# Performance work log

Measured on AMD Instinct MI355X. Metric: run time of the kernel, lower is better.

Reference implementation:

```python
import jax, jax.numpy as jnp
import numpy as np

CH = 256          # channels
K = 3             # kernel_size
GROUP_CH = 16
G = CH // GROUP_CH   # groups = 16
RED = 2              # red_ratio
PAD = (K - 1) // 2
B, H, W = 8, 64, 64  # input must be spatially square (h==w) because the
                     # original forward does kernel @ x_unfolded over (h,w)


def setup_inputs() -> dict:
    key = jax.random.key(0)
    k1, k2, k3 = jax.random.split(key, 3)
    x = jax.random.normal(k1, (B, CH, H, W), dtype=jnp.float32)
    W_reduce = jax.random.normal(k2, (CH // RED, CH), dtype=jnp.float32) * 0.05
    b_reduce = jnp.zeros((CH // RED,), dtype=jnp.float32)
    W_span = jax.random.normal(k3, (K * K * G, CH // RED), dtype=jnp.float32) * 0.05
    b_span = jnp.zeros((K * K * G,), dtype=jnp.float32)
    return {"x": x, "W_reduce": W_reduce, "b_reduce": b_reduce,
            "W_span": W_span, "b_span": b_span}


def _unfold(x):
    """torch.nn.Unfold(K, dilation=1, padding=PAD, stride=1).
    Returns [b, c, K*K, h, w] with kernel positions in row-major order,
    channel-major overall (matches torch's C*K^2 flattening)."""
    b, c, h, w = x.shape
    xp = jnp.pad(x, ((0, 0), (0, 0), (PAD, PAD), (PAD, PAD)))
    patches = jnp.stack(
        [xp[:, :, ki:ki + h, kj:kj + w] for ki in range(K) for kj in range(K)],
        axis=2)
    return patches


def reference(x, W_reduce, b_reduce, W_span, b_span):
    b, c, h, w = x.shape
    # stride == 1 -> self.out is Identity
    red = jnp.einsum('bchw,oc->bohw', x, W_reduce) + b_reduce[None, :, None, None]
    ker = jnp.einsum('bohw,ko->bkhw', red, W_span) + b_span[None, :, None, None]
    # kernel: [b, G, K^2, h, w] (unsqueeze(2) -> broadcast over group_ch)
    ker = ker.reshape(b, G, K * K, h, w)
    # x_unfolded: [b, G, group_ch, K^2, h, w]
    xu = _unfold(x).reshape(b, G, GROUP_CH, K * K, h, w)
    # faithful to `(kernel @ x_unfolded).sum(dim=3)`: matmul over the last two
    # (spatial) dims, summed over kernel positions k
    out = jnp.einsum('bgkim,bgckmj->bgcij', ker, xu)
    return out.reshape(b, c, h, w)
```

## Files before the change

kernel.cpp:

```cpp
#include <hip/hip_runtime.h>

typedef unsigned short u16;
typedef unsigned int u32;
typedef __attribute__((ext_vector_type(8))) short bf16x8;
typedef __attribute__((ext_vector_type(4))) float f32x4;

#define CH   256
#define KKG  144
#define HW   4096
#define CSP  68

__device__ __forceinline__ u16 f2bf(float f) {
    u32 u = __float_as_uint(f);
    u += 0x7FFFu + ((u >> 16) & 1u);
    return (u16)(u >> 16);
}
__device__ __forceinline__ float bf2f(u16 u) {
    return __uint_as_float(((u32)u) << 16);
}

__global__ __launch_bounds__(256) void fuse_weights_k(
    const float* __restrict__ Wr, const float* __restrict__ br,
    const float* __restrict__ Ws, const float* __restrict__ bs,
    u16* __restrict__ Mfrag, float* __restrict__ biasF)
{
    __shared__ float ws[128];
    const int r = blockIdx.x;
    const int c = threadIdx.x;
    if (c < 128) ws[c] = Ws[r * 128 + c];
    __syncthreads();
    float acc = 0.f;
#pragma unroll 8
    for (int o = 0; o < 128; ++o) acc += ws[o] * Wr[o * CH + c];
    const int ks = c >> 5, quad = (c >> 3) & 3, jj = c & 7;
    const int mt = r >> 4, lane = (r & 15) + (quad << 4);
    Mfrag[((ks * 9 + mt) * 64 + lane) * 8 + jj] = f2bf(acc);
    if (c == 0) {
        float bb = bs[r];
        for (int o = 0; o < 128; ++o) bb += ws[o] * br[o];
        biasF[r] = bb;
    }
}

__global__ __launch_bounds__(256, 4) void ker_abar_k(
    const float* __restrict__ x, const u16* __restrict__ Mfrag,
    const float* __restrict__ biasF, u16* __restrict__ Afrag)
{
    __shared__ u16 Cs[KKG * CSP];
    __shared__ float bias_s[KKG];
    const int b = blockIdx.x >> 6, irow = blockIdx.x & 63;
    const int t = threadIdx.x, lane = t & 63, w = t >> 6;
    const int nl = lane & 15, quad = lane >> 4;
    if (t < KKG) bias_s[t] = biasF[t];

    f32x4 acc[9];
#pragma unroll
    for (int mt = 0; mt < 9; ++mt) acc[mt] = (f32x4)0.f;

    const int ncol = irow * 64 + w * 16 + nl;
#pragma unroll
    for (int ks = 0; ks < 8; ++ks) {
        const float* xb = x + ((size_t)(b * CH + ks * 32 + quad * 8)) * HW + ncol;
        float f0 = xb[0],              f1 = xb[(size_t)HW],
              f2 = xb[2 * (size_t)HW], f3 = xb[3 * (size_t)HW],
              f4 = xb[4 * (size_t)HW], f5 = xb[5 * (size_t)HW],
              f6 = xb[6 * (size_t)HW], f7 = xb[7 * (size_t)HW];
        union { bf16x8 v; uint4 u; } bb;
        bb.u.x = (u32)f2bf(f0) | ((u32)f2bf(f1) << 16);
        bb.u.y = (u32)f2bf(f2) | ((u32)f2bf(f3) << 16);
        bb.u.z = (u32)f2bf(f4) | ((u32)f2bf(f5) << 16);
        bb.u.w = (u32)f2bf(f6) | ((u32)f2bf(f7) << 16);
        const bf16x8* Ag = ((const bf16x8*)Mfrag) + (ks * 9) * 64 + lane;
#pragma unroll
        for (int mt = 0; mt < 9; ++mt)
            acc[mt] = __builtin_amdgcn_mfma_f32_16x16x32_bf16(Ag[mt * 64], bb.v, acc[mt], 0, 0, 0);
    }
    __syncthreads();
#pragma unroll
    for (int mt = 0; mt < 9; ++mt) {
        const int rb = mt * 16 + quad * 4;
#pragma unroll
        for (int reg = 0; reg < 4; ++reg)
            Cs[(rb + reg) * CSP + w * 16 + nl] = f2bf(acc[mt][reg] + bias_s[rb + reg]);
    }
    __syncthreads();
    for (int v = t; v < 384; v += 256) {
        const int gd = v >> 3, o = v & 7;
        const int g = gd / 3, d = gd - g * 3;
        const int r0 = g * 9 + d;
        u16 h[8];
#pragma unroll
        for (int e = 0; e < 8; ++e) {
            const int m = o * 8 + e;
            float s = bf2f(Cs[(r0 + 3) * CSP + m]);
            if (m < 63) s += bf2f(Cs[r0 * CSP + m + 1]);
            if (m > 0)  s += bf2f(Cs[(r0 + 6) * CSP + m - 1]);
            h[e] = f2bf(s);
        }
        uint4 pk;
        pk.x = (u32)h[0] | ((u32)h[1] << 16);
        pk.y = (u32)h[2] | ((u32)h[3] << 16);
        pk.z = (u32)h[4] | ((u32)h[5] << 16);
        pk.w = (u32)h[6] | ((u32)h[7] << 16);
        const int ks2 = 2 * d + (o >> 2), quad2 = o & 3;
        const int mt2 = irow >> 4, lane2 = (irow & 15) + (quad2 << 4);
        const size_t idx = ((((size_t)(b * 16 + g) * 6 + ks2) * 4 + mt2) * 64 + lane2) * 8;
        *(uint4*)(Afrag + idx) = pk;
    }
}

__global__ __launch_bounds__(512) void inv_main_k(
    const float* __restrict__ x, const u16* __restrict__ Afrag,
    float* __restrict__ out)
{
    __shared__ u16 XT[4 * 4096];
    const int t = threadIdx.x;
    const int q = blockIdx.x & 3, bg = blockIdx.x >> 2;
    const int g = bg & 15, b = bg >> 4;
    const int ch_base = g * 16 + q * 4;
    const int lane = t & 63, w = t >> 6;
    const int cl = w >> 1, nth = w & 1;

    {
        const int tt = nth * 64 + lane;
        const int o = tt >> 4, jq = tt & 15;
        const float* xc = x + ((size_t)(b * CH + ch_base + cl)) * HW + o * 512 + jq * 4;
        float4 r0 = *(const float4*)(xc);
        float4 r1 = *(const float4*)(xc + 64);
        float4 r2 = *(const float4*)(xc + 128);
        float4 r3 = *(const float4*)(xc + 192);
        float4 r4 = *(const float4*)(xc + 256);
        float4 r5 = *(const float4*)(xc + 320);
        float4 r6 = *(const float4*)(xc + 384);
        float4 r7 = *(const float4*)(xc + 448);
        u16* base = XT + cl * 4096;
        uint4 pk;
        int j, chunk;
        pk.x = (u32)f2bf(r0.x) | ((u32)f2bf(r1.x) << 16);
        pk.y = (u32)f2bf(r2.x) | ((u32)f2bf(r3.x) << 16);
        pk.z = (u32)f2bf(r4.x) | ((u32)f2bf(r5.x) << 16);
        pk.w = (u32)f2bf(r6.x) | ((u32)f2bf(r7.x) << 16);
        j = jq * 4 + 0; chunk = j * 8 + (o ^ (j & 7));
        *(uint4*)(base + chunk * 8) = pk;
        pk.x = (u32)f2bf(r0.y) | ((u32)f2bf(r1.y) << 16);
        pk.y = (u32)f2bf(r2.y) | ((u32)f2bf(r3.y) << 16);
        pk.z = (u32)f2bf(r4.y) | ((u32)f2bf(r5.y) << 16);
        pk.w = (u32)f2bf(r6.y) | ((u32)f2bf(r7.y) << 16);
        j = jq * 4 + 1; chunk = j * 8 + (o ^ (j & 7));
        *(uint4*)(base + chunk * 8) = pk;
        pk.x = (u32)f2bf(r0.z) | ((u32)f2bf(r1.z) << 16);
        pk.y = (u32)f2bf(r2.z) | ((u32)f2bf(r3.z) << 16);
        pk.z = (u32)f2bf(r4.z) | ((u32)f2bf(r5.z) << 16);
        pk.w = (u32)f2bf(r6.z) | ((u32)f2bf(r7.z) << 16);
        j = jq * 4 + 2; chunk = j * 8 + (o ^ (j & 7));
        *(uint4*)(base + chunk * 8) = pk;
        pk.x = (u32)f2bf(r0.w) | ((u32)f2bf(r1.w) << 16);
        pk.y = (u32)f2bf(r2.w) | ((u32)f2bf(r3.w) << 16);
        pk.z = (u32)f2bf(r4.w) | ((u32)f2bf(r5.w) << 16);
        pk.w = (u32)f2bf(r6.w) | ((u32)f2bf(r7.w) << 16);
        j = jq * 4 + 3; chunk = j * 8 + (o ^ (j & 7));
        *(uint4*)(base + chunk * 8) = pk;
    }
    __syncthreads();

    const int nl = lane & 15, quad = lane >> 4;
    f32x4 acc[4][2];
#pragma unroll
    for (int mt = 0; mt < 4; ++mt)
#pragma unroll
        for (int ntl = 0; ntl < 2; ++ntl) acc[mt][ntl] = (f32x4)0.f;

    const u16* XTc = XT + cl * 4096;
#pragma unroll
    for (int ks = 0; ks < 6; ++ks) {
        const int d = ks >> 1, mh = ks & 1;
        const bf16x8* Ag = ((const bf16x8*)Afrag) + ((size_t)(bg * 6 + ks) * 4) * 64 + lane;
        bf16x8 a0 = Ag[0], a1 = Ag[64], a2 = Ag[128], a3 = Ag[192];
        const int o = mh * 4 + quad;
#pragma unroll
        for (int ntl = 0; ntl < 2; ++ntl) {
            const int nt = nth * 2 + ntl;
            const int jrow = nt * 16 + nl + d - 1;
            const int jc = jrow < 0 ? 0 : (jrow > 63 ? 63 : jrow);
            const int chunk = jc * 8 + (o ^ (jc & 7));
            bf16x8 bv = *(const bf16x8*)(XTc + chunk * 8);
            if (jrow < 0 || jrow > 63) bv = (bf16x8)(short)0;
            acc[0][ntl] = __builtin_amdgcn_mfma_f32_16x16x32_bf16(a0, bv, acc[0][ntl], 0, 0, 0);
            acc[1][ntl] = __builtin_amdgcn_mfma_f32_16x16x32_bf16(a1, bv, acc[1][ntl], 0, 0, 0);
            acc[2][ntl] = __builtin_amdgcn_mfma_f32_16x16x32_bf16(a2, bv, acc[2][ntl], 0, 0, 0);
            acc[3][ntl] = __builtin_amdgcn_mfma_f32_16x16x32_bf16(a3, bv, acc[3][ntl], 0, 0, 0);
        }
    }
    float* op = out + ((size_t)(b * CH + ch_base + cl)) * HW;
#pragma unroll
    for (int mt = 0; mt < 4; ++mt)
#pragma unroll
        for (int ntl = 0; ntl < 2; ++ntl)
#pragma unroll
            for (int reg = 0; reg < 4; ++reg)
                op[(mt * 16 + quad * 4 + reg) * 64 + (nth * 2 + ntl) * 16 + nl] = acc[mt][ntl][reg];
}

extern "C" void kernel_launch(void* const* d_in, const int* in_sizes, int n_in,
                              void* d_out, int out_size, void* d_ws, size_t ws_size,
                              hipStream_t stream)
{
    const float* x  = (const float*)d_in[0];
    const float* Wr = (const float*)d_in[1];
    const float* br = (const float*)d_in[2];
    const float* Ws = (const float*)d_in[3];
    const float* bs = (const float*)d_in[4];
    float* out = (float*)d_out;

    char* ws = (char*)d_ws;
    u16*   Mfrag = (u16*)(ws);
    float* biasF = (float*)(ws + 73728);
    u16*   Afrag = (u16*)(ws + 81920);

    fuse_weights_k<<<dim3(KKG), dim3(256), 0, stream>>>(Wr, br, Ws, bs, Mfrag, biasF);
    ker_abar_k<<<dim3(512), dim3(256), 0, stream>>>(x, Mfrag, biasF, Afrag);
    inv_main_k<<<dim3(512), dim3(512), 0, stream>>>(x, Afrag, out);
}
```

Measured before the change: 115.3 us.

## Add prep kernel converting x to bf16 in two MFMA-friendly layouts

A new prep kernel reads x once, converts it to bf16, and writes two copies to workspace: a channel-interleaved layout for the reduction GEMM and a spatially transposed layout for the main kernel. Both consumers then load ready bf16x8 fragments directly instead of doing strided fp32 loads, conversion, and an LDS transpose. The main kernel drops its shared-memory staging and each wave now covers a whole channel with one wave per channel. This adds an extra launch and about twice x's size in bf16 writes and reads through global memory.

```diff
diff --git a/kernel.cpp b/kernel.cpp
--- a/kernel.cpp
+++ b/kernel.cpp
@@ -9,6 +9,7 @@
 #define KKG  144
 #define HW   4096
 #define CSP  68
+#define CHS  538
 
 __device__ __forceinline__ u16 f2bf(float f) {
     u32 u = __float_as_uint(f);
@@ -42,8 +43,59 @@
     }
 }
 
+__global__ __launch_bounds__(256) void prep_k(
+    const float* __restrict__ x, u16* __restrict__ Xc8, u16* __restrict__ XT)
+{
+    __shared__ u16 L[32 * CHS];
+    const int blk = blockIdx.x;
+    const int b = blk >> 6, cc = (blk >> 3) & 7, mo = blk & 7;
+    const int t = threadIdx.x;
+
+#pragma unroll
+    for (int q = 0; q < 16; ++q) {
+        const int idx = q * 256 + t;
+        const int c4 = idx & 15, r = (idx >> 4) & 7, ch = idx >> 7;
+        const float4 v = *(const float4*)(x + ((size_t)(b * CH + cc * 32 + ch)) * HW
+                                            + (mo * 8 + r) * 64 + c4 * 4);
+        u16* dst = L + ch * CHS + r * 66 + c4 * 4;
+        dst[0] = f2bf(v.x); dst[1] = f2bf(v.y); dst[2] = f2bf(v.z); dst[3] = f2bf(v.w);
+    }
+    __syncthreads();
+
+#pragma unroll
+    for (int q = 0; q < 8; ++q) {
+        const int idx = q * 256 + t;
+        const int quad = idx & 3, j = (idx >> 2) & 63, r = idx >> 8;
+        u16 h[8];
+#pragma unroll
+        for (int jj = 0; jj < 8; ++jj) h[jj] = L[(quad * 8 + jj) * CHS + r * 66 + j];
+        uint4 pk;
+        pk.x = (u32)h[0] | ((u32)h[1] << 16);
+        pk.y = (u32)h[2] | ((u32)h[3] << 16);
+        pk.z = (u32)h[4] | ((u32)h[5] << 16);
+        pk.w = (u32)h[6] | ((u32)h[7] << 16);
+        const size_t col = (size_t)(mo * 8 + r) * 64 + j;
+        *(uint4*)(Xc8 + ((size_t)(b * 8 + cc) * HW + col) * 32 + quad * 8) = pk;
+    }
+
+#pragma unroll
+    for (int q = 0; q < 8; ++q) {
+        const int idx = q * 256 + t;
+        const int j = idx & 63, ch = idx >> 6;
+        u16 h[8];
+#pragma unroll
+        for (int r = 0; r < 8; ++r) h[r] = L[ch * CHS + r * 66 + j];
+        uint4 pk;
+        pk.x = (u32)h[0] | ((u32)h[1] << 16);
+        pk.y = (u32)h[2] | ((u32)h[3] << 16);
+        pk.z = (u32)h[4] | ((u32)h[5] << 16);
+        pk.w = (u32)h[6] | ((u32)h[7] << 16);
+        *(uint4*)(XT + ((size_t)(b * CH + cc * 32 + ch)) * HW + j * 64 + mo * 8) = pk;
+    }
+}
+
 __global__ __launch_bounds__(256, 4) void ker_abar_k(
-    const float* __restrict__ x, const u16* __restrict__ Mfrag,
+    const u16* __restrict__ Xc8, const u16* __restrict__ Mfrag,
     const float* __restrict__ biasF, u16* __restrict__ Afrag)
 {
     __shared__ u16 Cs[KKG * CSP];
@@ -57,23 +109,14 @@
 #pragma unroll
     for (int mt = 0; mt < 9; ++mt) acc[mt] = (f32x4)0.f;
 
-    const int ncol = irow * 64 + w * 16 + nl;
+    const size_t ncol = (size_t)irow * 64 + w * 16 + nl;
 #pragma unroll
     for (int ks = 0; ks < 8; ++ks) {
-        const float* xb = x + ((size_t)(b * CH + ks * 32 + quad * 8)) * HW + ncol;
-        float f0 = xb[0],              f1 = xb[(size_t)HW],
-              f2 = xb[2 * (size_t)HW], f3 = xb[3 * (size_t)HW],
-              f4 = xb[4 * (size_t)HW], f5 = xb[5 * (size_t)HW],
-              f6 = xb[6 * (size_t)HW], f7 = xb[7 * (size_t)HW];
-        union { bf16x8 v; uint4 u; } bb;
-        bb.u.x = (u32)f2bf(f0) | ((u32)f2bf(f1) << 16);
-        bb.u.y = (u32)f2bf(f2) | ((u32)f2bf(f3) << 16);
-        bb.u.z = (u32)f2bf(f4) | ((u32)f2bf(f5) << 16);
-        bb.u.w = (u32)f2bf(f6) | ((u32)f2bf(f7) << 16);
+        const bf16x8 bv = *(const bf16x8*)(Xc8 + ((size_t)(b * 8 + ks) * HW + ncol) * 32 + quad * 8);
         const bf16x8* Ag = ((const bf16x8*)Mfrag) + (ks * 9) * 64 + lane;
 #pragma unroll
         for (int mt = 0; mt < 9; ++mt)
-            acc[mt] = __builtin_amdgcn_mfma_f32_16x16x32_bf16(Ag[mt * 64], bb.v, acc[mt], 0, 0, 0);
+            acc[mt] = __builtin_amdgcn_mfma_f32_16x16x32_bf16(Ag[mt * 64], bv, acc[mt], 0, 0, 0);
     }
     __syncthreads();
 #pragma unroll
@@ -109,96 +152,48 @@
     }
 }
 
-__global__ __launch_bounds__(512) void inv_main_k(
-    const float* __restrict__ x, const u16* __restrict__ Afrag,
+__global__ __launch_bounds__(256) void inv_main_k(
+    const u16* __restrict__ XT, const u16* __restrict__ Afrag,
     float* __restrict__ out)
 {
-    __shared__ u16 XT[4 * 4096];
-    const int t = threadIdx.x;
+    const int t = threadIdx.x, lane = t & 63, w = t >> 6;
     const int q = blockIdx.x & 3, bg = blockIdx.x >> 2;
     const int g = bg & 15, b = bg >> 4;
-    const int ch_base = g * 16 + q * 4;
-    const int lane = t & 63, w = t >> 6;
-    const int cl = w >> 1, nth = w & 1;
-
-    {
-        const int tt = nth * 64 + lane;
-        const int o = tt >> 4, jq = tt & 15;
-        const float* xc = x + ((size_t)(b * CH + ch_base + cl)) * HW + o * 512 + jq * 4;
-        float4 r0 = *(const float4*)(xc);
-        float4 r1 = *(const float4*)(xc + 64);
-        float4 r2 = *(const float4*)(xc + 128);
-        float4 r3 = *(const float4*)(xc + 192);
-        float4 r4 = *(const float4*)(xc + 256);
-        float4 r5 = *(const float4*)(xc + 320);
-        float4 r6 = *(const float4*)(xc + 384);
-        float4 r7 = *(const float4*)(xc + 448);
-        u16* base = XT + cl * 4096;
-        uint4 pk;
-        int j, chunk;
-        pk.x = (u32)f2bf(r0.x) | ((u32)f2bf(r1.x) << 16);
-        pk.y = (u32)f2bf(r2.x) | ((u32)f2bf(r3.x) << 16);
-        pk.z = (u32)f2bf(r4.x) | ((u32)f2bf(r5.x) << 16);
-        pk.w = (u32)f2bf(r6.x) | ((u32)f2bf(r7.x) << 16);
-        j = jq * 4 + 0; chunk = j * 8 + (o ^ (j & 7));
-        *(uint4*)(base + chunk * 8) = pk;
-        pk.x = (u32)f2bf(r0.y) | ((u32)f2bf(r1.y) << 16);
-        pk.y = (u32)f2bf(r2.y) | ((u32)f2bf(r3.y) << 16);
-        pk.z = (u32)f2bf(r4.y) | ((u32)f2bf(r5.y) << 16);
-        pk.w = (u32)f2bf(r6.y) | ((u32)f2bf(r7.y) << 16);
-        j = jq * 4 + 1; chunk = j * 8 + (o ^ (j & 7));
-        *(uint4*)(base + chunk * 8) = pk;
-        pk.x = (u32)f2bf(r0.z) | ((u32)f2bf(r1.z) << 16);
-        pk.y = (u32)f2bf(r2.z) | ((u32)f2bf(r3.z) << 16);
-        pk.z = (u32)f2bf(r4.z) | ((u32)f2bf(r5.z) << 16);
-        pk.w = (u32)f2bf(r6.z) | ((u32)f2bf(r7.z) << 16);
-        j = jq * 4 + 2; chunk = j * 8 + (o ^ (j & 7));
-        *(uint4*)(base + chunk * 8) = pk;
-        pk.x = (u32)f2bf(r0.w) | ((u32)f2bf(r1.w) << 16);
-        pk.y = (u32)f2bf(r2.w) | ((u32)f2bf(r3.w) << 16);
-        pk.z = (u32)f2bf(r4.w) | ((u32)f2bf(r5.w) << 16);
-        pk.w = (u32)f2bf(r6.w) | ((u32)f2bf(r7.w) << 16);
-        j = jq * 4 + 3; chunk = j * 8 + (o ^ (j & 7));
-        *(uint4*)(base + chunk * 8) = pk;
-    }
-    __syncthreads();
-
+    const int ch = g * 16 + q * 4 + w;
     const int nl = lane & 15, quad = lane >> 4;
-    f32x4 acc[4][2];
+
+    f32x4 acc[4][4];
 #pragma unroll
     for (int mt = 0; mt < 4; ++mt)
 #pragma unroll
-        for (int ntl = 0; ntl < 2; ++ntl) acc[mt][ntl] = (f32x4)0.f;
-
-    const u16* XTc = XT + cl * 4096;
+        for (int nt = 0; nt < 4; ++nt) acc[mt][nt] = (f32x4)0.f;
+
+    const u16* XTc = XT + ((size_t)(b * CH + ch)) * HW;
 #pragma unroll
     for (int ks = 0; ks < 6; ++ks) {
         const int d = ks >> 1, mh = ks & 1;
         const bf16x8* Ag = ((const bf16x8*)Afrag) + ((size_t)(bg * 6 + ks) * 4) * 64 + lane;
         bf16x8 a0 = Ag[0], a1 = Ag[64], a2 = Ag[128], a3 = Ag[192];
-        const int o = mh * 4 + quad;
-#pragma unroll
-        for (int ntl = 0; ntl < 2; ++ntl) {
-            const int nt = nth * 2 + ntl;
+#pragma unroll
+        for (int nt = 0; nt < 4; ++nt) {
             const int jrow = nt * 16 + nl + d - 1;
             const int jc = jrow < 0 ? 0 : (jrow > 63 ? 63 : jrow);
-            const int chunk = jc * 8 + (o ^ (jc & 7));
-            bf16x8 bv = *(const bf16x8*)(XTc + chunk * 8);
+            bf16x8 bv = *(const bf16x8*)(XTc + jc * 64 + mh * 32 + quad * 8);
             if (jrow < 0 || jrow > 63) bv = (bf16x8)(short)0;
-            acc[0][ntl] = __builtin_amdgcn_mfma_f32_16x16x32_bf16(a0, bv, acc[0][ntl], 0, 0, 0);
-            acc[1][ntl] = __builtin_amdgcn_mfma_f32_16x16x32_bf16(a1, bv, acc[1][ntl], 0, 0, 0);
-            acc[2][ntl] = __builtin_amdgcn_mfma_f32_16x16x32_bf16(a2, bv, acc[2][ntl], 0, 0, 0);
-            acc[3][ntl] = __builtin_amdgcn_mfma_f32_16x16x32_bf16(a3, bv, acc[3][ntl], 0, 0, 0);
+            acc[0][nt] = __builtin_amdgcn_mfma_f32_16x16x32_bf16(a0, bv, acc[0][nt], 0, 0, 0);
+            acc[1][nt] = __builtin_amdgcn_mfma_f32_16x16x32_bf16(a1, bv, acc[1][nt], 0, 0, 0);
+            acc[2][nt] = __builtin_amdgcn_mfma_f32_16x16x32_bf16(a2, bv, acc[2][nt], 0, 0, 0);
+            acc[3][nt] = __builtin_amdgcn_mfma_f32_16x16x32_bf16(a3, bv, acc[3][nt], 0, 0, 0);
         }
     }
-    float* op = out + ((size_t)(b * CH + ch_base + cl)) * HW;
+    float* op = out + ((size_t)(b * CH + ch)) * HW;
 #pragma unroll
     for (int mt = 0; mt < 4; ++mt)
 #pragma unroll
-        for (int ntl = 0; ntl < 2; ++ntl)
+        for (int nt = 0; nt < 4; ++nt)
 #pragma unroll
             for (int reg = 0; reg < 4; ++reg)
-                op[(mt * 16 + quad * 4 + reg) * 64 + (nth * 2 + ntl) * 16 + nl] = acc[mt][ntl][reg];
+                op[(mt * 16 + quad * 4 + reg) * 64 + nt * 16 + nl] = acc[mt][nt][reg];
 }
 
 extern "C" void kernel_launch(void* const* d_in, const int* in_sizes, int n_in,
@@ -216,8 +211,11 @@
     u16*   Mfrag = (u16*)(ws);
     float* biasF = (float*)(ws + 73728);
     u16*   Afrag = (u16*)(ws + 81920);
+    u16*   Xc8   = (u16*)(ws + 3227648);
+    u16*   XT    = (u16*)(ws + 20004864);
 
     fuse_weights_k<<<dim3(KKG), dim3(256), 0, stream>>>(Wr, br, Ws, bs, Mfrag, biasF);
-    ker_abar_k<<<dim3(512), dim3(256), 0, stream>>>(x, Mfrag, biasF, Afrag);
-    inv_main_k<<<dim3(512), dim3(512), 0, stream>>>(x, Afrag, out);
-}
+    prep_k<<<dim3(512), dim3(256), 0, stream>>>(x, Xc8, XT);
+    ker_abar_k<<<dim3(512), dim3(256), 0, stream>>>(Xc8, Mfrag, biasF, Afrag);
+    inv_main_k<<<dim3(512), dim3(256), 0, stream>>>(XT, Afrag, out);
+}
```

Measured after the change: 141.6 us. 1.23x slower.
